# Kernel optimization log

Measured on AMD Instinct MI355X. Metric: run time of the kernel, lower is better.

## Reference

```python
import jax, jax.numpy as jnp
import numpy as np

D_K = 32
N_HEADS = 16


def setup_inputs() -> dict:
    key = jax.random.key(0)
    ks = jax.random.split(key, 11)
    B, S, F = 32, 2048, 128
    d_k, d_v, filt = 32, 32, 3
    return {
        "q_in": jax.random.normal(ks[0], (B, S, F), jnp.float32),
        "k_in": jax.random.normal(ks[1], (B, S, F), jnp.float32),
        "v_in": jax.random.normal(ks[2], (B, S, F), jnp.float32),
        "Wq": jax.random.normal(ks[3], (F, d_k), jnp.float32) * 0.05,
        "bq": jax.random.normal(ks[4], (d_k,), jnp.float32) * 0.05,
        "Wk": jax.random.normal(ks[5], (F, d_k), jnp.float32) * 0.05,
        "bk": jax.random.normal(ks[6], (d_k,), jnp.float32) * 0.05,
        "Wv": jax.random.normal(ks[7], (F, d_v), jnp.float32) * 0.05,
        "bv": jax.random.normal(ks[8], (d_v,), jnp.float32) * 0.05,
        "Wo": jax.random.normal(ks[9], (N_HEADS * d_v, filt), jnp.float32) * 0.05,
        "bo": jax.random.normal(ks[10], (filt,), jnp.float32) * 0.05,
    }


def reference(q_in, k_in, v_in, Wq, bq, Wk, bk, Wv, bv, Wo, bo):
    # SingleAttention: Dense projections then scaled dot-product attention.
    q = q_in @ Wq + bq            # [B,S,d_k]
    k = k_in @ Wk + bk            # [B,S,d_k]
    v = v_in @ Wv + bv            # [B,S,d_v]
    scores = jnp.einsum('bqd,bkd->bqk', q, k) / jnp.sqrt(jnp.float32(D_K))
    attn = jax.nn.softmax(scores, axis=-1)
    head = jnp.einsum('bqk,bkd->bqd', attn, v)  # [B,S,d_v]
    # Original uses [SingleAttention()]*n_heads -> all heads are the SAME layer,
    # so the concat is n_heads identical copies of one head output.
    combined = jnp.tile(head, (1, 1, N_HEADS))   # [B,S,n_heads*d_v]
    return combined @ Wo + bo                    # [B,S,filter_size]
```

## Files before the change

kernel.cpp:

```cpp
#include <hip/hip_runtime.h>
#include <stdint.h>

using f16 = _Float16;
typedef _Float16 f16x8 __attribute__((ext_vector_type(8)));
typedef float f32x4 __attribute__((ext_vector_type(4)));

constexpr int Bn    = 32;
constexpr int Sn    = 2048;
constexpr int Fn    = 128;
constexpr int DKn   = 32;
constexpr int NHn   = 16;
constexpr int FILTn = 3;
constexpr int Mn    = Bn * Sn;

constexpr float QSCALE = 0.1767766952966369f * 1.4426950408889634f;

constexpr int MISC_WOEFF = 0;
constexpr int MISC_BO    = 96;
constexpr int MISC_BQ    = 99;
constexpr int MISC_BK    = 131;
constexpr int MISC_BV    = 163;

#define ASYNC_COPY16(gp, lp)                                                   \
    __builtin_amdgcn_global_load_lds(                                          \
        (const __attribute__((address_space(1))) uint32_t*)(const void*)(gp),  \
        (__attribute__((address_space(3))) uint32_t*)(lp), 16, 0, 0)

#define WAIT_VM2 __builtin_amdgcn_s_waitcnt(0xF72)
#define WAIT_VM0 __builtin_amdgcn_s_waitcnt(0xF70)

__global__ __launch_bounds__(256) void prep_kernel(
    const float* __restrict__ Wq, const float* __restrict__ bq,
    const float* __restrict__ Wk, const float* __restrict__ bk,
    const float* __restrict__ Wv, const float* __restrict__ bv,
    const float* __restrict__ Wo, const float* __restrict__ bo,
    f16* __restrict__ wtg, float* __restrict__ misc)
{
    for (int idx = blockIdx.x * 256 + threadIdx.x; idx < 3 * 4096;
         idx += gridDim.x * 256) {
        const int T    = idx >> 12;
        const int r    = idx & 4095;
        const int nt   = r >> 11;
        const int ks   = (r >> 9) & 3;
        const int lane = (r >> 3) & 63;
        const int j    = r & 7;
        const int k    = ks * 32 + (lane >> 4) * 8 + j;
        const int c    = nt * 16 + (lane & 15);
        const float* W = (T == 0) ? Wq : ((T == 1) ? Wk : Wv);
        const float sc = (T == 0) ? QSCALE : 1.0f;
        wtg[idx] = (f16)(W[k * DKn + c] * sc);
    }
    if (blockIdx.x == 0) {
        const int t = threadIdx.x;
        if (t < 96) {
            const int d = t / 3, f = t - 3 * d;
            float s = 0.f;
#pragma unroll
            for (int h = 0; h < NHn; ++h) s += Wo[(h * DKn + d) * FILTn + f];
            misc[MISC_WOEFF + t] = s;
        } else if (t < 99) {
            misc[MISC_BO + (t - 96)] = bo[t - 96];
        } else if (t < 131) {
            misc[MISC_BQ + (t - 99)] = bq[t - 99] * QSCALE;
        } else if (t < 163) {
            misc[MISC_BK + (t - 131)] = bk[t - 131];
        } else if (t < 195) {
            misc[MISC_BV + (t - 163)] = bv[t - 163];
        }
    }
}

__global__ __launch_bounds__(256) void qkv_proj(
    const float* __restrict__ q_in, const float* __restrict__ k_in,
    const float* __restrict__ v_in,
    const f16* __restrict__ wtg, const float* __restrict__ misc,
    f16* __restrict__ q_ws, f16* __restrict__ k_ws, f16* __restrict__ v_ws)
{
    const int t    = threadIdx.x;
    const int w    = t >> 6;
    const int lane = t & 63;
    const int n    = lane & 15;
    const int quad = lane >> 4;
    const int T    = blockIdx.x / 512;
    const int rowA = (((blockIdx.x - T * 512) * 4 + w)) * 32;
    const int rowB = rowA + 16;
    const float* in = (T == 0) ? q_in : ((T == 1) ? k_in : v_in);

    f16x8 wf[2][4];
#pragma unroll
    for (int nt = 0; nt < 2; ++nt)
#pragma unroll
        for (int ks = 0; ks < 4; ++ks)
            wf[nt][ks] =
                *(const f16x8*)(wtg + T * 4096 + (nt * 4 + ks) * 512 + lane * 8);

    f16x8 afA[4], afB[4];
#pragma unroll
    for (int ks = 0; ks < 4; ++ks) {
        const float* pA = in + (size_t)(rowA + n) * Fn + ks * 32 + quad * 8;
        const float* pB = in + (size_t)(rowB + n) * Fn + ks * 32 + quad * 8;
        const float4 a0 = *(const float4*)pA;
        const float4 a1 = *(const float4*)(pA + 4);
        const float4 b0 = *(const float4*)pB;
        const float4 b1 = *(const float4*)(pB + 4);
        f16x8 a, b;
        a[0]=(f16)a0.x; a[1]=(f16)a0.y; a[2]=(f16)a0.z; a[3]=(f16)a0.w;
        a[4]=(f16)a1.x; a[5]=(f16)a1.y; a[6]=(f16)a1.z; a[7]=(f16)a1.w;
        b[0]=(f16)b0.x; b[1]=(f16)b0.y; b[2]=(f16)b0.z; b[3]=(f16)b0.w;
        b[4]=(f16)b1.x; b[5]=(f16)b1.y; b[6]=(f16)b1.z; b[7]=(f16)b1.w;
        afA[ks] = a;
        afB[ks] = b;
    }

    if (T < 2) {
        const float* bb = misc + (T == 0 ? MISC_BQ : MISC_BK);
        const float b0 = bb[n], b1 = bb[16 + n];
        f32x4 accA0 = {b0, b0, b0, b0}, accA1 = {b1, b1, b1, b1};
        f32x4 accB0 = {b0, b0, b0, b0}, accB1 = {b1, b1, b1, b1};
#pragma unroll
        for (int ks = 0; ks < 4; ++ks) {
            accA0 = __builtin_amdgcn_mfma_f32_16x16x32_f16(afA[ks], wf[0][ks], accA0, 0, 0, 0);
            accA1 = __builtin_amdgcn_mfma_f32_16x16x32_f16(afA[ks], wf[1][ks], accA1, 0, 0, 0);
            accB0 = __builtin_amdgcn_mfma_f32_16x16x32_f16(afB[ks], wf[0][ks], accB0, 0, 0, 0);
            accB1 = __builtin_amdgcn_mfma_f32_16x16x32_f16(afB[ks], wf[1][ks], accB1, 0, 0, 0);
        }
        f16* ows = (T == 0) ? q_ws : k_ws;
#pragma unroll
        for (int r = 0; r < 4; ++r) {
            const int ra = rowA + quad * 4 + r;
            const int rb = rowB + quad * 4 + r;
            ows[(size_t)ra * DKn + n]      = (f16)accA0[r];
            ows[(size_t)ra * DKn + 16 + n] = (f16)accA1[r];
            ows[(size_t)rb * DKn + n]      = (f16)accB0[r];
            ows[(size_t)rb * DKn + 16 + n] = (f16)accB1[r];
        }
    } else {
        f32x4 accA0 = {0.f,0.f,0.f,0.f}, accA1 = {0.f,0.f,0.f,0.f};
        f32x4 accB0 = {0.f,0.f,0.f,0.f}, accB1 = {0.f,0.f,0.f,0.f};
#pragma unroll
        for (int ks = 0; ks < 4; ++ks) {
            accA0 = __builtin_amdgcn_mfma_f32_16x16x32_f16(wf[0][ks], afA[ks], accA0, 0, 0, 0);
            accA1 = __builtin_amdgcn_mfma_f32_16x16x32_f16(wf[1][ks], afA[ks], accA1, 0, 0, 0);
            accB0 = __builtin_amdgcn_mfma_f32_16x16x32_f16(wf[0][ks], afB[ks], accB0, 0, 0, 0);
            accB1 = __builtin_amdgcn_mfma_f32_16x16x32_f16(wf[1][ks], afB[ks], accB1, 0, 0, 0);
        }
        const int b  = rowA >> 11;
        const int sA = (rowA & (Sn - 1)) + n;
        const int sB = sA + 16;
#pragma unroll
        for (int r = 0; r < 4; ++r) {
            const int d0 = quad * 4 + r;
            v_ws[((size_t)(b * DKn + d0)) * Sn + sA] =
                (f16)(accA0[r] + misc[MISC_BV + d0]);
            v_ws[((size_t)(b * DKn + 16 + d0)) * Sn + sA] =
                (f16)(accA1[r] + misc[MISC_BV + 16 + d0]);
            v_ws[((size_t)(b * DKn + d0)) * Sn + sB] =
                (f16)(accB0[r] + misc[MISC_BV + d0]);
            v_ws[((size_t)(b * DKn + 16 + d0)) * Sn + sB] =
                (f16)(accB1[r] + misc[MISC_BV + 16 + d0]);
        }
    }
}

__global__ __launch_bounds__(256, 4) void flash_mfma(
    const f16* __restrict__ q_ws, const f16* __restrict__ k_ws,
    const f16* __restrict__ v_ws,
    const float* __restrict__ misc, float* __restrict__ out)
{
    __shared__ f16 kv[3][2][2048];
    __shared__ f16 psh[4 * 16 * 64];

    const int t    = threadIdx.x;
    const int w    = t >> 6;
    const int lane = t & 63;
    const int n    = lane & 15;
    const int quad = lane >> 4;
    const int b    = (blockIdx.x & 7) * 4 + (blockIdx.x >> 8);
    const int qt   = (blockIdx.x >> 3) & 31;

    const f16* Ksrc = k_ws + (size_t)b * Sn * DKn
                    + (size_t)(t >> 2) * DKn + (((t & 3) ^ ((t >> 3) & 3)) * 8);
    const f16* Vsrc = v_ws + (size_t)b * DKn * Sn
                    + (size_t)(t >> 3) * Sn + (((t & 7) ^ ((t >> 3) & 7)) * 8);

#define STAGE(KT, BUF)                                              \
    {                                                               \
        ASYNC_COPY16(Ksrc + (size_t)(KT) * 2048, &kv[BUF][0][w * 512]); \
        ASYNC_COPY16(Vsrc + (size_t)(KT) * 64,   &kv[BUF][1][w * 512]); \
    }

    const int qrow0 = b * Sn + qt * 64 + w * 16;
    const f16x8 qa = *(const f16x8*)(q_ws + (size_t)(qrow0 + n) * DKn + quad * 8);

    int koff[4];
#pragma unroll
    for (int g = 0; g < 4; ++g)
        koff[g] = (g * 64 + n * 4 + (quad ^ ((n >> 1) & 3))) * 8;
    int voff[2][2];
#pragma unroll
    for (int ks = 0; ks < 2; ++ks) {
        voff[0][ks] = (n * 8 + ((ks * 4 + quad) ^ (n & 7))) * 8;
        voff[1][ks] = ((16 + n) * 8 + ((ks * 4 + quad) ^ (n & 7))) * 8;
    }

    f16* pw = psh + w * 16 * 64;
    const f16* prd0 = pw + n * 64 + ((quad ^ (n & 7)) << 3);
    const f16* prd1 = pw + n * 64 + (((4 + quad) ^ (n & 7)) << 3);
    int pwo[16];
#pragma unroll
    for (int r = 0; r < 4; ++r) {
        const int row = quad * 4 + r;
#pragma unroll
        for (int g = 0; g < 4; ++g)
            pwo[r * 4 + g] =
                row * 64 + (((g * 2 + (n >> 3)) ^ (row & 7)) << 3) + (n & 7);
    }

    f32x4 o0 = {0.f, 0.f, 0.f, 0.f};
    f32x4 o1 = {0.f, 0.f, 0.f, 0.f};
    float l[4] = {0.f, 0.f, 0.f, 0.f};
    const f32x4 zero = {0.f, 0.f, 0.f, 0.f};

    STAGE(0, 0)
    STAGE(1, 1)

#pragma unroll 1
    for (int kt = 0; kt < Sn / 64; ++kt) {
        const int cur = kt % 3;
        WAIT_VM2;
        __builtin_amdgcn_s_barrier();
        STAGE((kt + 2) & 31, (kt + 2) % 3)

        const f16* Kt = &kv[cur][0][0];
        const f16* Vt = &kv[cur][1][0];

        const f16x8 kb0 = *(const f16x8*)(Kt + koff[0]);
        const f16x8 kb1 = *(const f16x8*)(Kt + koff[1]);
        const f16x8 kb2 = *(const f16x8*)(Kt + koff[2]);
        const f16x8 kb3 = *(const f16x8*)(Kt + koff[3]);
        const f16x8 va0 = *(const f16x8*)(Vt + voff[0][0]);
        const f16x8 va1 = *(const f16x8*)(Vt + voff[0][1]);
        const f16x8 va2 = *(const f16x8*)(Vt + voff[1][0]);
        const f16x8 va3 = *(const f16x8*)(Vt + voff[1][1]);

        const f32x4 s0 = __builtin_amdgcn_mfma_f32_16x16x32_f16(qa, kb0, zero, 0, 0, 0);
        const f32x4 s1 = __builtin_amdgcn_mfma_f32_16x16x32_f16(qa, kb1, zero, 0, 0, 0);
        const f32x4 s2 = __builtin_amdgcn_mfma_f32_16x16x32_f16(qa, kb2, zero, 0, 0, 0);
        const f32x4 s3 = __builtin_amdgcn_mfma_f32_16x16x32_f16(qa, kb3, zero, 0, 0, 0);

#pragma unroll
        for (int r = 0; r < 4; ++r) {
            const float p0 = __builtin_amdgcn_exp2f(s0[r]);
            const float p1 = __builtin_amdgcn_exp2f(s1[r]);
            const float p2 = __builtin_amdgcn_exp2f(s2[r]);
            const float p3 = __builtin_amdgcn_exp2f(s3[r]);
            l[r] += (p0 + p1) + (p2 + p3);
            pw[pwo[r * 4 + 0]] = (f16)p0;
            pw[pwo[r * 4 + 1]] = (f16)p1;
            pw[pwo[r * 4 + 2]] = (f16)p2;
            pw[pwo[r * 4 + 3]] = (f16)p3;
        }

        const f16x8 pa0 = *(const f16x8*)prd0;
        const f16x8 pa1 = *(const f16x8*)prd1;
        o0 = __builtin_amdgcn_mfma_f32_16x16x32_f16(pa0, va0, o0, 0, 0, 0);
        o0 = __builtin_amdgcn_mfma_f32_16x16x32_f16(pa1, va1, o0, 0, 0, 0);
        o1 = __builtin_amdgcn_mfma_f32_16x16x32_f16(pa0, va2, o1, 0, 0, 0);
        o1 = __builtin_amdgcn_mfma_f32_16x16x32_f16(pa1, va3, o1, 0, 0, 0);
    }
#undef STAGE
    WAIT_VM0;

#pragma unroll
    for (int r = 0; r < 4; ++r) {
        float v = l[r];
        v += __shfl_xor(v, 1, 16);
        v += __shfl_xor(v, 2, 16);
        v += __shfl_xor(v, 4, 16);
        v += __shfl_xor(v, 8, 16);
        l[r] = v;
    }

    float w0f[FILTn], w1f[FILTn];
#pragma unroll
    for (int f = 0; f < FILTn; ++f) {
        w0f[f] = misc[MISC_WOEFF + n * FILTn + f];
        w1f[f] = misc[MISC_WOEFF + (16 + n) * FILTn + f];
    }
#pragma unroll
    for (int r = 0; r < 4; ++r) {
        const float inv = 1.f / l[r];
        const float a0 = o0[r] * inv;
        const float a1 = o1[r] * inv;
#pragma unroll
        for (int f = 0; f < FILTn; ++f) {
            float v = a0 * w0f[f] + a1 * w1f[f];
            v += __shfl_xor(v, 1, 16);
            v += __shfl_xor(v, 2, 16);
            v += __shfl_xor(v, 4, 16);
            v += __shfl_xor(v, 8, 16);
            if (n == f) {
                const int row = qrow0 + quad * 4 + r;
                out[(size_t)row * FILTn + f] = v + misc[MISC_BO + f];
            }
        }
    }
}

extern "C" void kernel_launch(void* const* d_in, const int* in_sizes, int n_in,
                              void* d_out, int out_size, void* d_ws,
                              size_t ws_size, hipStream_t stream)
{
    const float* q_in = (const float*)d_in[0];
    const float* k_in = (const float*)d_in[1];
    const float* v_in = (const float*)d_in[2];
    const float* Wq   = (const float*)d_in[3];
    const float* bq   = (const float*)d_in[4];
    const float* Wk   = (const float*)d_in[5];
    const float* bk   = (const float*)d_in[6];
    const float* Wv   = (const float*)d_in[7];
    const float* bv   = (const float*)d_in[8];
    const float* Wo   = (const float*)d_in[9];
    const float* bo   = (const float*)d_in[10];
    float* out = (float*)d_out;

    f16*   ws   = (f16*)d_ws;
    f16*   q_ws = ws;
    f16*   k_ws = ws + (size_t)Mn * DKn;
    f16*   v_ws = ws + 2 * (size_t)Mn * DKn;
    f16*   wtg  = ws + 3 * (size_t)Mn * DKn;
    float* misc = (float*)(wtg + 3 * 4096);

    prep_kernel<<<16, 256, 0, stream>>>(Wq, bq, Wk, bk, Wv, bv, Wo, bo, wtg, misc);

    qkv_proj<<<3 * 512, 256, 0, stream>>>(
        q_in, k_in, v_in, wtg, misc, q_ws, k_ws, v_ws);

    flash_mfma<<<Bn * (Sn / 64), 256, 0, stream>>>(
        q_ws, k_ws, v_ws, misc, out);
}
```

Baseline: 185.8 us.

## Compute transposed scores so P stays in registers, dropping LDS round-trip

Swaps the MFMA operands so each lane holds scores for one query column across keys. The exp2 results then map directly into the A operand of 16x16x16 MFMAs for the PV product, with no LDS write and read-back of P. The V fragment loads change to 4-wide reads to match, and the row-sum reduction moves to cross-quad shuffles plus a broadcast at the end. This removes per-tile LDS stores and loads of the probability matrix and frees LDS, at the cost of twice as many smaller MFMAs and more V load instructions.

Result: faster. 174.3 us (-6.2%).

```diff
diff --git a/kernel.cpp b/kernel.cpp
--- a/kernel.cpp
+++ b/kernel.cpp
@@ -3,6 +3,7 @@
 
 using f16 = _Float16;
 typedef _Float16 f16x8 __attribute__((ext_vector_type(8)));
+typedef _Float16 f16x4 __attribute__((ext_vector_type(4)));
 typedef float f32x4 __attribute__((ext_vector_type(4)));
 
 constexpr int Bn    = 32;
@@ -168,7 +169,6 @@
     const float* __restrict__ misc, float* __restrict__ out)
 {
     __shared__ f16 kv[3][2][2048];
-    __shared__ f16 psh[4 * 16 * 64];
 
     const int t    = threadIdx.x;
     const int w    = t >> 6;
@@ -196,29 +196,20 @@
 #pragma unroll
     for (int g = 0; g < 4; ++g)
         koff[g] = (g * 64 + n * 4 + (quad ^ ((n >> 1) & 3))) * 8;
-    int voff[2][2];
-#pragma unroll
-    for (int ks = 0; ks < 2; ++ks) {
-        voff[0][ks] = (n * 8 + ((ks * 4 + quad) ^ (n & 7))) * 8;
-        voff[1][ks] = ((16 + n) * 8 + ((ks * 4 + quad) ^ (n & 7))) * 8;
-    }
-
-    f16* pw = psh + w * 16 * 64;
-    const f16* prd0 = pw + n * 64 + ((quad ^ (n & 7)) << 3);
-    const f16* prd1 = pw + n * 64 + (((4 + quad) ^ (n & 7)) << 3);
-    int pwo[16];
-#pragma unroll
-    for (int r = 0; r < 4; ++r) {
-        const int row = quad * 4 + r;
-#pragma unroll
-        for (int g = 0; g < 4; ++g)
-            pwo[r * 4 + g] =
-                row * 64 + (((g * 2 + (n >> 3)) ^ (row & 7)) << 3) + (n & 7);
-    }
+
+    int voff2[2][4];
+#pragma unroll
+    for (int h = 0; h < 2; ++h)
+#pragma unroll
+        for (int s = 0; s < 4; ++s) {
+            const int d  = h * 16 + n;
+            const int jc = s * 2 + (quad >> 1);
+            voff2[h][s] = (d * 8 + (jc ^ (d & 7))) * 8 + (quad & 1) * 4;
+        }
 
     f32x4 o0 = {0.f, 0.f, 0.f, 0.f};
     f32x4 o1 = {0.f, 0.f, 0.f, 0.f};
-    float l[4] = {0.f, 0.f, 0.f, 0.f};
+    float lsum = 0.f;
     const f32x4 zero = {0.f, 0.f, 0.f, 0.f};
 
     STAGE(0, 0)
@@ -238,48 +229,44 @@
         const f16x8 kb1 = *(const f16x8*)(Kt + koff[1]);
         const f16x8 kb2 = *(const f16x8*)(Kt + koff[2]);
         const f16x8 kb3 = *(const f16x8*)(Kt + koff[3]);
-        const f16x8 va0 = *(const f16x8*)(Vt + voff[0][0]);
-        const f16x8 va1 = *(const f16x8*)(Vt + voff[0][1]);
-        const f16x8 va2 = *(const f16x8*)(Vt + voff[1][0]);
-        const f16x8 va3 = *(const f16x8*)(Vt + voff[1][1]);
-
-        const f32x4 s0 = __builtin_amdgcn_mfma_f32_16x16x32_f16(qa, kb0, zero, 0, 0, 0);
-        const f32x4 s1 = __builtin_amdgcn_mfma_f32_16x16x32_f16(qa, kb1, zero, 0, 0, 0);
-        const f32x4 s2 = __builtin_amdgcn_mfma_f32_16x16x32_f16(qa, kb2, zero, 0, 0, 0);
-        const f32x4 s3 = __builtin_amdgcn_mfma_f32_16x16x32_f16(qa, kb3, zero, 0, 0, 0);
-
-#pragma unroll
-        for (int r = 0; r < 4; ++r) {
-            const float p0 = __builtin_amdgcn_exp2f(s0[r]);
-            const float p1 = __builtin_amdgcn_exp2f(s1[r]);
-            const float p2 = __builtin_amdgcn_exp2f(s2[r]);
-            const float p3 = __builtin_amdgcn_exp2f(s3[r]);
-            l[r] += (p0 + p1) + (p2 + p3);
-            pw[pwo[r * 4 + 0]] = (f16)p0;
-            pw[pwo[r * 4 + 1]] = (f16)p1;
-            pw[pwo[r * 4 + 2]] = (f16)p2;
-            pw[pwo[r * 4 + 3]] = (f16)p3;
-        }
-
-        const f16x8 pa0 = *(const f16x8*)prd0;
-        const f16x8 pa1 = *(const f16x8*)prd1;
-        o0 = __builtin_amdgcn_mfma_f32_16x16x32_f16(pa0, va0, o0, 0, 0, 0);
-        o0 = __builtin_amdgcn_mfma_f32_16x16x32_f16(pa1, va1, o0, 0, 0, 0);
-        o1 = __builtin_amdgcn_mfma_f32_16x16x32_f16(pa0, va2, o1, 0, 0, 0);
-        o1 = __builtin_amdgcn_mfma_f32_16x16x32_f16(pa1, va3, o1, 0, 0, 0);
+        f16x4 vb[2][4];
+#pragma unroll
+        for (int h = 0; h < 2; ++h)
+#pragma unroll
+            for (int s = 0; s < 4; ++s)
+                vb[h][s] = *(const f16x4*)(Vt + voff2[h][s]);
+
+        const f32x4 s0 = __builtin_amdgcn_mfma_f32_16x16x32_f16(kb0, qa, zero, 0, 0, 0);
+        const f32x4 s1 = __builtin_amdgcn_mfma_f32_16x16x32_f16(kb1, qa, zero, 0, 0, 0);
+        const f32x4 s2 = __builtin_amdgcn_mfma_f32_16x16x32_f16(kb2, qa, zero, 0, 0, 0);
+        const f32x4 s3 = __builtin_amdgcn_mfma_f32_16x16x32_f16(kb3, qa, zero, 0, 0, 0);
+
+        f16x4 pa[4];
+#pragma unroll
+        for (int g = 0; g < 4; ++g) {
+            const f32x4 sg = (g == 0) ? s0 : ((g == 1) ? s1 : ((g == 2) ? s2 : s3));
+            const float p0 = __builtin_amdgcn_exp2f(sg[0]);
+            const float p1 = __builtin_amdgcn_exp2f(sg[1]);
+            const float p2 = __builtin_amdgcn_exp2f(sg[2]);
+            const float p3 = __builtin_amdgcn_exp2f(sg[3]);
+            lsum += (p0 + p1) + (p2 + p3);
+            f16x4 pp;
+            pp[0] = (f16)p0; pp[1] = (f16)p1; pp[2] = (f16)p2; pp[3] = (f16)p3;
+            pa[g] = pp;
+        }
+
+#pragma unroll
+        for (int s = 0; s < 4; ++s) {
+            o0 = __builtin_amdgcn_mfma_f32_16x16x16f16(pa[s], vb[0][s], o0, 0, 0, 0);
+            o1 = __builtin_amdgcn_mfma_f32_16x16x16f16(pa[s], vb[1][s], o1, 0, 0, 0);
+        }
     }
 #undef STAGE
     WAIT_VM0;
 
-#pragma unroll
-    for (int r = 0; r < 4; ++r) {
-        float v = l[r];
-        v += __shfl_xor(v, 1, 16);
-        v += __shfl_xor(v, 2, 16);
-        v += __shfl_xor(v, 4, 16);
-        v += __shfl_xor(v, 8, 16);
-        l[r] = v;
-    }
+    float lf = lsum;
+    lf += __shfl_xor(lf, 16);
+    lf += __shfl_xor(lf, 32);
 
     float w0f[FILTn], w1f[FILTn];
 #pragma unroll
@@ -289,7 +276,7 @@
     }
 #pragma unroll
     for (int r = 0; r < 4; ++r) {
-        const float inv = 1.f / l[r];
+        const float inv = 1.f / __shfl(lf, quad * 4 + r);
         const float a0 = o0[r] * inv;
         const float a1 = o1[r] * inv;
 #pragma unroll
```
